# Performance work log

Hardware: AMD Instinct MI355X
Metric: run time of the kernel (lower is better)

Reference implementation:

```python
import jax, jax.numpy as jnp
import numpy as np

B, T, C, H = 2, 2048, 1024, 16
HD = C // H  # head dim = 64


def setup_inputs() -> dict:
    key = jax.random.key(0)
    ks = jax.random.split(key, 9)
    s = 1.0 / np.sqrt(C)
    return {
        "x": jax.random.normal(ks[0], (B, T, C), dtype=jnp.float32),
        "Wq": jax.random.normal(ks[1], (C, C), dtype=jnp.float32) * s,
        "bq": jax.random.normal(ks[2], (C,), dtype=jnp.float32) * 0.02,
        "Wk": jax.random.normal(ks[3], (C, C), dtype=jnp.float32) * s,
        "bk": jax.random.normal(ks[4], (C,), dtype=jnp.float32) * 0.02,
        "Wv": jax.random.normal(ks[5], (C, C), dtype=jnp.float32) * s,
        "bv": jax.random.normal(ks[6], (C,), dtype=jnp.float32) * 0.02,
        "Wo": jax.random.normal(ks[7], (C, C), dtype=jnp.float32) * s,
        "bo": jax.random.normal(ks[8], (C,), dtype=jnp.float32) * 0.02,
    }


def reference(x, Wq, bq, Wk, bk, Wv, bv, Wo, bo):
    # Projections (torch Linear: x @ W.T + b; here W stored pre-transposed as [C_in, C_out])
    q = x @ Wq + bq  # (B,T,C)
    k = x @ Wk + bk
    v = x @ Wv + bv
    # Split heads: (B,T,C) -> (B,H,T,HD)
    q = q.reshape(B, T, H, HD).transpose(0, 2, 1, 3)
    k = k.reshape(B, T, H, HD).transpose(0, 2, 1, 3)
    v = v.reshape(B, T, H, HD).transpose(0, 2, 1, 3)
    # NOTE: original module never applies a causal mask despite its name.
    score = jnp.einsum("bhqd,bhkd->bhqk", q, k) / jnp.sqrt(jnp.float32(HD))
    score = jax.nn.softmax(score, axis=-1)
    y = jnp.einsum("bhqk,bhkd->bhqd", score, v)
    y = y.transpose(0, 2, 1, 3).reshape(B, T, C)
    # dropout is identity in eval mode
    return y @ Wo + bo
```

## Files before the change

### kernel.cpp

```cpp
#include <hip/hip_runtime.h>
#include <math.h>

#define B_ 2
#define T_ 2048
#define C_ 1024
#define H_ 16
#define HD_ 64
#define M_ (B_*T_)

typedef _Float16 half2v __attribute__((ext_vector_type(2)));
typedef _Float16 half4v __attribute__((ext_vector_type(4)));
typedef _Float16 half8v __attribute__((ext_vector_type(8)));
typedef float f32x4 __attribute__((ext_vector_type(4)));

#define GLD_LDS(gp, lp) \
  __builtin_amdgcn_global_load_lds( \
      (const __attribute__((address_space(1))) void*)(gp), \
      (__attribute__((address_space(3))) void*)(lp), 16, 0, 0)

__global__ __launch_bounds__(256) void prep_kernel(
    const float* __restrict__ x,
    const float* __restrict__ Wq, const float* __restrict__ Wk,
    const float* __restrict__ Wv, const float* __restrict__ Wo,
    const float* __restrict__ bq, const float* __restrict__ bk,
    const float* __restrict__ bv,
    _Float16* __restrict__ xh, _Float16* __restrict__ Wt3,
    _Float16* __restrict__ Wot, float* __restrict__ b3)
{
  __shared__ float tile[32][33];
  const int blk = blockIdx.x, thr = threadIdx.x;
  if (blk < 4096) {
    int i = blk * 256 + thr;
    float4 v = ((const float4*)x)[i];
    half4v h; h[0] = (_Float16)v.x; h[1] = (_Float16)v.y;
    h[2] = (_Float16)v.z; h[3] = (_Float16)v.w;
    ((half4v*)xh)[i] = h;
  } else if (blk < 8192) {
    int zz = (blk - 4096) >> 10;
    int bxy = (blk - 4096) & 1023;
    const float* W; _Float16* Wt;
    switch (zz) {
      case 0:  W = Wq; Wt = Wt3; break;
      case 1:  W = Wk; Wt = Wt3 + (size_t)1024 * 1024; break;
      case 2:  W = Wv; Wt = Wt3 + (size_t)2048 * 1024; break;
      default: W = Wo; Wt = Wot; break;
    }
    const int n0 = (bxy & 31) * 32, k0 = (bxy >> 5) * 32;
    const int tx = thr & 31, ty = thr >> 5;
#pragma unroll
    for (int r = 0; r < 4; r++) {
      int k = ty + r * 8;
      tile[k][tx] = W[(size_t)(k0 + k) * C_ + n0 + tx];
    }
    __syncthreads();
#pragma unroll
    for (int r = 0; r < 4; r++) {
      int n = ty + r * 8;
      Wt[(size_t)(n0 + n) * C_ + k0 + tx] = (_Float16)tile[tx][n];
    }
  } else {
    int i = (blk - 8192) * 256 + thr;
    const float* s = (i < 1024) ? bq : ((i < 2048) ? bk : bv);
    b3[i] = s[i & 1023];
  }
}

template <int BM, int BN, int EPI>
__global__ __launch_bounds__(256) void gemm_f16_kernel(
    const _Float16* __restrict__ A, const _Float16* __restrict__ Bw,
    const float* __restrict__ bias,
    _Float16* __restrict__ o0, _Float16* __restrict__ o1,
    _Float16* __restrict__ o2, float* __restrict__ of)
{
  constexpr int FM = BM / 32, FN = BN / 32;
  __shared__ __align__(16) _Float16 As[BM * 32];
  __shared__ __align__(16) _Float16 Bs[BN * 32];
  const int t = threadIdx.x;
  const int w = t >> 6, lane = t & 63, l15 = lane & 15, quad = lane >> 4;
  const int wm = (w & 1) * (BM / 2), wn = (w >> 1) * (BN / 2);
  const int bm = blockIdx.y * BM, bn = blockIdx.x * BN;
  const int lrow = lane >> 2, lcol = (lane & 3) * 8;

  f32x4 acc[FM][FN];
#pragma unroll
  for (int i = 0; i < FM; i++)
#pragma unroll
    for (int j = 0; j < FN; j++) acc[i][j] = (f32x4){0.f, 0.f, 0.f, 0.f};

  for (int k0 = 0; k0 < 1024; k0 += 32) {
#pragma unroll
    for (int i = 0; i < BM / 64; i++) {
      int ca = w + 4 * i;
      int row = ca * 16 + lrow;
      GLD_LDS(A + (size_t)(bm + row) * 1024 + k0 + lcol, As + ca * 512);
    }
#pragma unroll
    for (int i = 0; i < BN / 64; i++) {
      int cb = w + 4 * i;
      int row = cb * 16 + lrow;
      GLD_LDS(Bw + (size_t)(bn + row) * 1024 + k0 + lcol, Bs + cb * 512);
    }
    __syncthreads();

    half8v af[FM], bf[FN];
#pragma unroll
    for (int mt = 0; mt < FM; mt++)
      af[mt] = *(const half8v*)(As + (wm + mt * 16 + l15) * 32 + quad * 8);
#pragma unroll
    for (int nt = 0; nt < FN; nt++)
      bf[nt] = *(const half8v*)(Bs + (wn + nt * 16 + l15) * 32 + quad * 8);
#pragma unroll
    for (int mt = 0; mt < FM; mt++)
#pragma unroll
      for (int nt = 0; nt < FN; nt++)
        acc[mt][nt] = __builtin_amdgcn_mfma_f32_16x16x32_f16(
            af[mt], bf[nt], acc[mt][nt], 0, 0, 0);
    __syncthreads();
  }

#pragma unroll
  for (int mt = 0; mt < FM; mt++)
#pragma unroll
    for (int nt = 0; nt < FN; nt++) {
      int n = bn + wn + nt * 16 + l15;
      float bv = bias[n];
      if (EPI == 0 && bn >= 2048) {
        int dg = n - 2048;
        int hh = dg >> 6, hd = dg & 63;
        int m0 = bm + wm + mt * 16 + quad * 4;
        int bb = m0 >> 11, tt = m0 & 2047;
        half2v p01 = __builtin_bit_cast(half2v,
            __builtin_amdgcn_cvt_pkrtz(acc[mt][nt][0] + bv, acc[mt][nt][1] + bv));
        half2v p23 = __builtin_bit_cast(half2v,
            __builtin_amdgcn_cvt_pkrtz(acc[mt][nt][2] + bv, acc[mt][nt][3] + bv));
        half4v pk = __builtin_shufflevector(p01, p23, 0, 1, 2, 3);
        *(half4v*)(o2 + (((size_t)(bb * H_ + hh) * 64 + hd) * 2048 + tt)) = pk;
      } else {
#pragma unroll
        for (int r = 0; r < 4; r++) {
          int m = bm + wm + mt * 16 + quad * 4 + r;
          float v = acc[mt][nt][r] + bv;
          if (EPI == 0) {
            if (bn < 1024) {
              o0[(size_t)m * 1024 + n] = (_Float16)(v * 0.180336884f);
            } else {
              o1[(size_t)m * 1024 + (n - 1024)] = (_Float16)v;
            }
          } else {
            of[(size_t)m * 1024 + n] = v;
          }
        }
      }
    }
}

__global__ __launch_bounds__(512) void attn_f16_kernel(
    const _Float16* __restrict__ Qh, const _Float16* __restrict__ Kh,
    const _Float16* __restrict__ Vt, _Float16* __restrict__ Yh)
{
  __shared__ __align__(16) _Float16 Ks[128 * 68];
  __shared__ __align__(16) _Float16 Vs[64 * 132];
  const int t = threadIdx.x;
  const int w = t >> 6, lane = t & 63, l15 = lane & 15, quad = lane >> 4;
  const int qt = blockIdx.x, h = blockIdx.y, b = blockIdx.z;
  const int qg = qt * 128 + w * 16 + l15;
  const size_t qoff = ((size_t)(b * T_ + qg)) * C_ + h * HD_;

  half8v qf[2];
  qf[0] = *(const half8v*)(Qh + qoff + quad * 8);
  qf[1] = *(const half8v*)(Qh + qoff + 32 + quad * 8);

  f32x4 o[4];
#pragma unroll
  for (int i = 0; i < 4; i++) o[i] = (f32x4){0.f, 0.f, 0.f, 0.f};
  float m_run = -INFINITY, l_run = 0.f;

  const size_t kbase = ((size_t)b * T_) * C_ + h * HD_;
  const size_t vbase = ((size_t)(b * H_ + h)) * HD_ * 2048;

  for (int kt0 = 0; kt0 < T_; kt0 += 128) {
#pragma unroll
    for (int i = 0; i < 2; i++) {
      int slot = t + i * 512;
      int row = slot >> 3, cp = slot & 7;
      *(uint4*)((char*)Ks + row * 136 + cp * 16) =
          *(const uint4*)(Kh + kbase + (size_t)(kt0 + row) * C_ + cp * 8);
    }
#pragma unroll
    for (int i = 0; i < 2; i++) {
      int slot = t + i * 512;
      int row = slot >> 4, cp = slot & 15;
      *(uint4*)((char*)Vs + row * 264 + cp * 16) =
          *(const uint4*)(Vt + vbase + (size_t)row * 2048 + kt0 + cp * 8);
    }
    __syncthreads();

    f32x4 s[8];
#pragma unroll
    for (int kt = 0; kt < 8; kt++) {
      s[kt] = (f32x4){0.f, 0.f, 0.f, 0.f};
      int key = kt * 16 + l15;
#pragma unroll
      for (int ks = 0; ks < 2; ks++) {
        half8v kf = *(const half8v*)((char*)Ks + key * 136 + (ks * 4 + quad) * 16);
        s[kt] = __builtin_amdgcn_mfma_f32_16x16x32_f16(kf, qf[ks], s[kt], 0, 0, 0);
      }
    }

    float tmax = -INFINITY;
#pragma unroll
    for (int kt = 0; kt < 8; kt++)
#pragma unroll
      for (int r = 0; r < 4; r++) tmax = fmaxf(tmax, s[kt][r]);
    tmax = fmaxf(tmax, __shfl_xor(tmax, 16));
    tmax = fmaxf(tmax, __shfl_xor(tmax, 32));
    float mnew = fmaxf(m_run, tmax);
    float alpha = __builtin_amdgcn_exp2f(m_run - mnew);

    float psum = 0.f;
    half4v pf[8];
#pragma unroll
    for (int kt = 0; kt < 8; kt++) {
      float p0 = __builtin_amdgcn_exp2f(s[kt][0] - mnew);
      float p1 = __builtin_amdgcn_exp2f(s[kt][1] - mnew);
      float p2 = __builtin_amdgcn_exp2f(s[kt][2] - mnew);
      float p3 = __builtin_amdgcn_exp2f(s[kt][3] - mnew);
      psum += (p0 + p1) + (p2 + p3);
      half2v pk01 = __builtin_bit_cast(half2v, __builtin_amdgcn_cvt_pkrtz(p0, p1));
      half2v pk23 = __builtin_bit_cast(half2v, __builtin_amdgcn_cvt_pkrtz(p2, p3));
      pf[kt] = __builtin_shufflevector(pk01, pk23, 0, 1, 2, 3);
    }
    psum += __shfl_xor(psum, 16);
    psum += __shfl_xor(psum, 32);
    l_run = l_run * alpha + psum;
    m_run = mnew;
#pragma unroll
    for (int dt = 0; dt < 4; dt++) o[dt] *= alpha;

#pragma unroll
    for (int dt = 0; dt < 4; dt++) {
      int d = dt * 16 + l15;
#pragma unroll
      for (int kt = 0; kt < 8; kt++) {
        half4v vf = *(const half4v*)((char*)Vs + d * 264 + kt * 32 + quad * 8);
        o[dt] = __builtin_amdgcn_mfma_f32_16x16x16f16(vf, pf[kt], o[dt], 0, 0, 0);
      }
    }
    __syncthreads();
  }

  float inv = 1.0f / l_run;
#pragma unroll
  for (int dt = 0; dt < 4; dt++) {
    half4v yv;
#pragma unroll
    for (int r = 0; r < 4; r++) yv[r] = (_Float16)(o[dt][r] * inv);
    *(half4v*)(Yh + qoff + dt * 16 + quad * 4) = yv;
  }
}

extern "C" void kernel_launch(void* const* d_in, const int* in_sizes, int n_in,
                              void* d_out, int out_size, void* d_ws, size_t ws_size,
                              hipStream_t stream) {
  const float* x  = (const float*)d_in[0];
  const float* Wq = (const float*)d_in[1];
  const float* bq = (const float*)d_in[2];
  const float* Wk = (const float*)d_in[3];
  const float* bk = (const float*)d_in[4];
  const float* Wv = (const float*)d_in[5];
  const float* bv = (const float*)d_in[6];
  const float* Wo = (const float*)d_in[7];
  const float* bo = (const float*)d_in[8];
  float* out = (float*)d_out;

  char* ws = (char*)d_ws;
  _Float16* xh   = (_Float16*)(ws);
  _Float16* Qh   = (_Float16*)(ws + (((size_t)8)  << 20));
  _Float16* Kh   = (_Float16*)(ws + (((size_t)16) << 20));
  _Float16* Vt   = (_Float16*)(ws + (((size_t)24) << 20));
  _Float16* Yh   = (_Float16*)(ws + (((size_t)32) << 20));
  _Float16* Wt3  = (_Float16*)(ws + (((size_t)40) << 20));
  _Float16* Wot  = (_Float16*)(ws + (((size_t)46) << 20));
  float*    b3   = (float*)   (ws + (((size_t)48) << 20));

  prep_kernel<<<8204, 256, 0, stream>>>(x, Wq, Wk, Wv, Wo, bq, bk, bv,
                                        xh, Wt3, Wot, b3);

  gemm_f16_kernel<128, 128, 0><<<dim3(24, 32), 256, 0, stream>>>(
      xh, Wt3, b3, Qh, Kh, Vt, nullptr);

  attn_f16_kernel<<<dim3(T_ / 128, H_, B_), 512, 0, stream>>>(Qh, Kh, Vt, Yh);

  gemm_f16_kernel<64, 128, 1><<<dim3(8, 64), 256, 0, stream>>>(
      Yh, Wot, bo, nullptr, nullptr, nullptr, out);
}
```

Measured before the change: 206.7 us.

## Double-buffer K/V tiles in attention with register prefetch of next tile

```diff
diff --git a/kernel.cpp b/kernel.cpp
--- a/kernel.cpp
+++ b/kernel.cpp
@@ -158,8 +158,8 @@
     const _Float16* __restrict__ Qh, const _Float16* __restrict__ Kh,
     const _Float16* __restrict__ Vt, _Float16* __restrict__ Yh)
 {
-  __shared__ __align__(16) _Float16 Ks[128 * 68];
-  __shared__ __align__(16) _Float16 Vs[64 * 132];
+  __shared__ __align__(16) _Float16 Ks[2][128 * 68];
+  __shared__ __align__(16) _Float16 Vs[2][64 * 132];
   const int t = threadIdx.x;
   const int w = t >> 6, lane = t & 63, l15 = lane & 15, quad = lane >> 4;
   const int qt = blockIdx.x, h = blockIdx.y, b = blockIdx.z;
@@ -178,22 +178,34 @@
   const size_t kbase = ((size_t)b * T_) * C_ + h * HD_;
   const size_t vbase = ((size_t)(b * H_ + h)) * HD_ * 2048;
 
-  for (int kt0 = 0; kt0 < T_; kt0 += 128) {
-#pragma unroll
-    for (int i = 0; i < 2; i++) {
-      int slot = t + i * 512;
-      int row = slot >> 3, cp = slot & 7;
-      *(uint4*)((char*)Ks + row * 136 + cp * 16) =
-          *(const uint4*)(Kh + kbase + (size_t)(kt0 + row) * C_ + cp * 8);
-    }
-#pragma unroll
-    for (int i = 0; i < 2; i++) {
-      int slot = t + i * 512;
-      int row = slot >> 4, cp = slot & 15;
-      *(uint4*)((char*)Vs + row * 264 + cp * 16) =
-          *(const uint4*)(Vt + vbase + (size_t)row * 2048 + kt0 + cp * 8);
-    }
+  const int ks0 = t, ks1 = t + 512;
+  const int krow0 = ks0 >> 3, kcp0 = ks0 & 7;
+  const int krow1 = ks1 >> 3, kcp1 = ks1 & 7;
+  const int vrow0 = ks0 >> 4, vcp0 = ks0 & 15;
+  const int vrow1 = ks1 >> 4, vcp1 = ks1 & 15;
+  const _Float16* kp0 = Kh + kbase + (size_t)krow0 * C_ + kcp0 * 8;
+  const _Float16* kp1 = Kh + kbase + (size_t)krow1 * C_ + kcp1 * 8;
+  const _Float16* vp0 = Vt + vbase + (size_t)vrow0 * 2048 + vcp0 * 8;
+  const _Float16* vp1 = Vt + vbase + (size_t)vrow1 * 2048 + vcp1 * 8;
+
+  uint4 kr0 = *(const uint4*)kp0, kr1 = *(const uint4*)kp1;
+  uint4 vr0 = *(const uint4*)vp0, vr1 = *(const uint4*)vp1;
+
+  for (int it = 0; it < 16; ++it) {
+    _Float16* Ksb = Ks[it & 1];
+    _Float16* Vsb = Vs[it & 1];
+    *(uint4*)((char*)Ksb + krow0 * 136 + kcp0 * 16) = kr0;
+    *(uint4*)((char*)Ksb + krow1 * 136 + kcp1 * 16) = kr1;
+    *(uint4*)((char*)Vsb + vrow0 * 264 + vcp0 * 16) = vr0;
+    *(uint4*)((char*)Vsb + vrow1 * 264 + vcp1 * 16) = vr1;
     __syncthreads();
+
+    if (it + 1 < 16) {
+      kp0 += 128 * (size_t)C_;  kp1 += 128 * (size_t)C_;
+      vp0 += 128;               vp1 += 128;
+      kr0 = *(const uint4*)kp0; kr1 = *(const uint4*)kp1;
+      vr0 = *(const uint4*)vp0; vr1 = *(const uint4*)vp1;
+    }
 
     f32x4 s[8];
 #pragma unroll
@@ -202,7 +214,7 @@
       int key = kt * 16 + l15;
 #pragma unroll
       for (int ks = 0; ks < 2; ks++) {
-        half8v kf = *(const half8v*)((char*)Ks + key * 136 + (ks * 4 + quad) * 16);
+        half8v kf = *(const half8v*)((char*)Ksb + key * 136 + (ks * 4 + quad) * 16);
         s[kt] = __builtin_amdgcn_mfma_f32_16x16x32_f16(kf, qf[ks], s[kt], 0, 0, 0);
       }
     }
@@ -242,11 +254,10 @@
       int d = dt * 16 + l15;
 #pragma unroll
       for (int kt = 0; kt < 8; kt++) {
-        half4v vf = *(const half4v*)((char*)Vs + d * 264 + kt * 32 + quad * 8);
+        half4v vf = *(const half4v*)((char*)Vsb + d * 264 + kt * 32 + quad * 8);
         o[dt] = __builtin_amdgcn_mfma_f32_16x16x16f16(vf, pf[kt], o[dt], 0, 0, 0);
       }
     }
-    __syncthreads();
   }
 
   float inv = 1.0f / l_run;
```

After: 308.4 us. 1.49x slower.

## Double-buffer K/V tiles in attention with register prefetch and one sync

Applied to the files above, without the earlier changes.

```diff
diff --git a/kernel.cpp b/kernel.cpp
--- a/kernel.cpp
+++ b/kernel.cpp
@@ -158,8 +158,8 @@
     const _Float16* __restrict__ Qh, const _Float16* __restrict__ Kh,
     const _Float16* __restrict__ Vt, _Float16* __restrict__ Yh)
 {
-  __shared__ __align__(16) _Float16 Ks[128 * 68];
-  __shared__ __align__(16) _Float16 Vs[64 * 132];
+  __shared__ __align__(16) _Float16 Ks[2][64 * 68];
+  __shared__ __align__(16) _Float16 Vs[2][64 * 68];
   const int t = threadIdx.x;
   const int w = t >> 6, lane = t & 63, l15 = lane & 15, quad = lane >> 4;
   const int qt = blockIdx.x, h = blockIdx.y, b = blockIdx.z;
@@ -178,38 +178,43 @@
   const size_t kbase = ((size_t)b * T_) * C_ + h * HD_;
   const size_t vbase = ((size_t)(b * H_ + h)) * HD_ * 2048;
 
-  for (int kt0 = 0; kt0 < T_; kt0 += 128) {
-#pragma unroll
-    for (int i = 0; i < 2; i++) {
-      int slot = t + i * 512;
-      int row = slot >> 3, cp = slot & 7;
-      *(uint4*)((char*)Ks + row * 136 + cp * 16) =
-          *(const uint4*)(Kh + kbase + (size_t)(kt0 + row) * C_ + cp * 8);
-    }
-#pragma unroll
-    for (int i = 0; i < 2; i++) {
-      int slot = t + i * 512;
-      int row = slot >> 4, cp = slot & 15;
-      *(uint4*)((char*)Vs + row * 264 + cp * 16) =
-          *(const uint4*)(Vt + vbase + (size_t)row * 2048 + kt0 + cp * 8);
-    }
+  const int srow = t >> 3, scp = t & 7;
+  const int lds_off = srow * 136 + scp * 16;
+  const _Float16* kp = Kh + kbase + (size_t)srow * C_ + scp * 8;
+  const _Float16* vp = Vt + vbase + (size_t)srow * 2048 + scp * 8;
+
+  uint4 kr = *(const uint4*)kp;
+  uint4 vr = *(const uint4*)vp;
+
+  for (int it = 0; it < 32; ++it) {
+    _Float16* Ksb = Ks[it & 1];
+    _Float16* Vsb = Vs[it & 1];
+    *(uint4*)((char*)Ksb + lds_off) = kr;
+    *(uint4*)((char*)Vsb + lds_off) = vr;
     __syncthreads();
 
-    f32x4 s[8];
-#pragma unroll
-    for (int kt = 0; kt < 8; kt++) {
+    if (it + 1 < 32) {
+      kp += (size_t)64 * C_;
+      vp += 64;
+      kr = *(const uint4*)kp;
+      vr = *(const uint4*)vp;
+    }
+
+    f32x4 s[4];
+#pragma unroll
+    for (int kt = 0; kt < 4; kt++) {
       s[kt] = (f32x4){0.f, 0.f, 0.f, 0.f};
       int key = kt * 16 + l15;
 #pragma unroll
       for (int ks = 0; ks < 2; ks++) {
-        half8v kf = *(const half8v*)((char*)Ks + key * 136 + (ks * 4 + quad) * 16);
+        half8v kf = *(const half8v*)((char*)Ksb + key * 136 + (ks * 4 + quad) * 16);
         s[kt] = __builtin_amdgcn_mfma_f32_16x16x32_f16(kf, qf[ks], s[kt], 0, 0, 0);
       }
     }
 
     float tmax = -INFINITY;
 #pragma unroll
-    for (int kt = 0; kt < 8; kt++)
+    for (int kt = 0; kt < 4; kt++)
 #pragma unroll
       for (int r = 0; r < 4; r++) tmax = fmaxf(tmax, s[kt][r]);
     tmax = fmaxf(tmax, __shfl_xor(tmax, 16));
@@ -218,9 +223,9 @@
     float alpha = __builtin_amdgcn_exp2f(m_run - mnew);
 
     float psum = 0.f;
-    half4v pf[8];
-#pragma unroll
-    for (int kt = 0; kt < 8; kt++) {
+    half4v pf[4];
+#pragma unroll
+    for (int kt = 0; kt < 4; kt++) {
       float p0 = __builtin_amdgcn_exp2f(s[kt][0] - mnew);
       float p1 = __builtin_amdgcn_exp2f(s[kt][1] - mnew);
       float p2 = __builtin_amdgcn_exp2f(s[kt][2] - mnew);
@@ -241,12 +246,11 @@
     for (int dt = 0; dt < 4; dt++) {
       int d = dt * 16 + l15;
 #pragma unroll
-      for (int kt = 0; kt < 8; kt++) {
-        half4v vf = *(const half4v*)((char*)Vs + d * 264 + kt * 32 + quad * 8);
+      for (int kt = 0; kt < 4; kt++) {
+        half4v vf = *(const half4v*)((char*)Vsb + d * 136 + kt * 32 + quad * 8);
         o[dt] = __builtin_amdgcn_mfma_f32_16x16x16f16(vf, pf[kt], o[dt], 0, 0, 0);
       }
     }
-    __syncthreads();
   }
 
   float inv = 1.0f / l_run;
```

New measurement: 305.1 us. 47.7% more time.
